# Kernel tuning notes

Measured on AMD Instinct MI355X. Metric: run time of the kernel, lower is better.

The kernel has to match this reference:

```python
import jax, jax.numpy as jnp
import numpy as np

N, T, L = 4, 2048, 2048
DQIN, DFEAT, DQK, DV = 32, 34, 64, 64  # modality feat=34 -> V input = 34-2 = 32, K input = last col


def _sorted_timeline(k, shape):
    return jnp.sort(jax.random.uniform(k, shape, jnp.float32) * 100.0, axis=-1)


def setup_inputs() -> dict:
    key = jax.random.key(0)
    ks = jax.random.split(key, 32)
    inp = {}
    inp["ref_data"] = jax.random.normal(ks[0], (N, 1, T, DQIN), jnp.float32)
    inp["ref_t"] = _sorted_timeline(ks[1], (N, 1, T))
    inp["m1_data"] = jax.random.normal(ks[2], (N, 1, L, DFEAT), jnp.float32)
    inp["m1_t"] = _sorted_timeline(ks[3], (N, 1, L))
    inp["m2_data"] = jax.random.normal(ks[4], (N, 1, L, DFEAT), jnp.float32)
    inp["m2_t"] = _sorted_timeline(ks[5], (N, 1, L))
    inp["m3_data"] = jax.random.normal(ks[6], (N, 1, L, DFEAT), jnp.float32)
    inp["m3_t"] = _sorted_timeline(ks[7], (N, 1, L))
    # shared W_Q (bias=False): d_q_in -> d_qk
    inp["Wq"] = jax.random.normal(ks[8], (DQIN, DQK), jnp.float32) / np.sqrt(DQIN)
    # per-modality params: W_K: 1 -> d_qk (with bias), W_V: (DFEAT-2) -> d_v (with bias), log-temperature
    for i, m in enumerate(["1", "2", "3"]):
        b = 9 + 4 * i
        inp["Wk" + m] = jax.random.normal(ks[b], (1, DQK), jnp.float32)
        inp["bk" + m] = jax.random.normal(ks[b + 1], (DQK,), jnp.float32) * 0.02
        inp["Wv" + m] = jax.random.normal(ks[b + 2], (DFEAT - 2, DV), jnp.float32) / np.sqrt(DFEAT - 2)
        inp["bv" + m] = jax.random.normal(ks[b + 3], (DV,), jnp.float32) * 0.02
        inp["log_tau" + m] = jnp.zeros((), jnp.float32)  # log(init_tau=1)
    return inp


def _unimodal(Q, ref_t, data, t, Wk, bk, Wv, bv, log_tau):
    # K path: last feature column through linear, then feature_map_k = [1, -x]
    Kr = data[..., -1:] @ Wk + bk                                   # (N,1,L,DQK)
    K = jnp.concatenate([jnp.ones(Kr.shape[:-1] + (1,), Kr.dtype), -Kr], axis=-1)  # (N,1,L,DQK+1)
    V = data[..., :-2] @ Wv + bv                                    # (N,1,L,DV)
    tau = jnp.exp(log_tau)
    # gaussian weight: -(Q.K)^2 / tau
    S = -jnp.square(jnp.einsum('nhtc,nhlc->nhtl', Q, K)) / tau       # (N,1,T,L)
    mask = (ref_t[..., :, None] >= t[..., None, :]).astype(S.dtype)  # (N,1,T,L)
    A = jax.nn.softmax(S * mask, axis=-1) * mask
    return jnp.einsum('nhtl,nhlc->nhtc', A, V)                       # (N,1,T,DV)


def reference(ref_data, ref_t, m1_data, m1_t, m2_data, m2_t, m3_data, m3_t,
              Wq, Wk1, bk1, Wv1, bv1, log_tau1, Wk2, bk2, Wv2, bv2, log_tau2,
              Wk3, bk3, Wv3, bv3, log_tau3):
    # compute_Q (qk_type='time'): Q = add_one(W_Q(ref_data)) -> append ones column
    Qr = jnp.einsum('nhtd,dk->nhtk', ref_data, Wq)
    Q = jnp.concatenate([Qr, jnp.ones(Qr.shape[:-1] + (1,), Qr.dtype)], axis=-1)  # (N,1,T,DQK+1)
    y1 = _unimodal(Q, ref_t, m1_data, m1_t, Wk1, bk1, Wv1, bv1, log_tau1)
    y2 = _unimodal(Q, ref_t, m2_data, m2_t, Wk2, bk2, Wv2, bv2, log_tau2)
    y3 = _unimodal(Q, ref_t, m3_data, m3_t, Wk3, bk3, Wv3, bv3, log_tau3)
    # original returns dict {m1: y1, m2: y2, m3: y3}; stacked here (3,N,1,T,DV)
    return jnp.stack([y1, y2, y3], axis=0)
```

## Files before the change

### kernel.cpp

```cpp
#include <hip/hip_runtime.h>

namespace {

typedef unsigned int uint;
typedef unsigned short ushort_t;
typedef __attribute__((ext_vector_type(8))) short bf16x8;
typedef __attribute__((ext_vector_type(4))) float f32x4;

constexpr int N = 4, T = 2048, L = 2048;
constexpr int DQIN = 32, DQK = 64;

constexpr int VI_SZ = 3 * N * 64 * L;
constexpr int X_SZ = 3 * N * L;
constexpr int A_SZ = 3 * N * T;

union PK8 { int i[4]; bf16x8 s; };

__global__ __launch_bounds__(256) void mm_prep(
    const float* __restrict__ ref_data, const float* __restrict__ ref_t,
    const float* __restrict__ d1, const float* __restrict__ t1,
    const float* __restrict__ d2, const float* __restrict__ t2,
    const float* __restrict__ d3, const float* __restrict__ t3,
    const float* __restrict__ Wq,
    const float* __restrict__ Wk1, const float* __restrict__ bk1,
    const float* __restrict__ Wv1, const float* __restrict__ bv1, const float* __restrict__ lt1,
    const float* __restrict__ Wk2, const float* __restrict__ bk2,
    const float* __restrict__ Wv2, const float* __restrict__ bv2, const float* __restrict__ lt2,
    const float* __restrict__ Wk3, const float* __restrict__ bk3,
    const float* __restrict__ Wv3, const float* __restrict__ bv3, const float* __restrict__ lt3,
    float* __restrict__ Aq, float* __restrict__ Gq, int* __restrict__ Cq,
    ushort_t* __restrict__ VI, float* __restrict__ X) {
  const int b = blockIdx.x;
  const int tid = threadIdx.x;

  if (b < 32) {
    __shared__ float sWq[DQIN * DQK];
    __shared__ float sWk[3][DQK];
    __shared__ float sbk[3][DQK];
    for (int i = tid; i < DQIN * DQK; i += 256) sWq[i] = Wq[i];
    if (tid < DQK) {
      sWk[0][tid] = Wk1[tid]; sWk[1][tid] = Wk2[tid]; sWk[2][tid] = Wk3[tid];
      sbk[0][tid] = bk1[tid]; sbk[1][tid] = bk2[tid]; sbk[2][tid] = bk3[tid];
    }
    __syncthreads();
    const int idx = b * 256 + tid;
    float x[DQIN];
    const float* rp = ref_data + idx * DQIN;
#pragma unroll
    for (int i = 0; i < DQIN; i++) x[i] = rp[i];
    float qr[DQK];
#pragma unroll
    for (int j = 0; j < DQK; j += 4) {
      float4 acc4 = make_float4(0.f, 0.f, 0.f, 0.f);
#pragma unroll
      for (int i = 0; i < DQIN; i++) {
        const float4 w = *(const float4*)&sWq[i * DQK + j];
        acc4.x = fmaf(x[i], w.x, acc4.x);
        acc4.y = fmaf(x[i], w.y, acc4.y);
        acc4.z = fmaf(x[i], w.z, acc4.z);
        acc4.w = fmaf(x[i], w.w, acc4.w);
      }
      qr[j] = acc4.x; qr[j + 1] = acc4.y; qr[j + 2] = acc4.z; qr[j + 3] = acc4.w;
    }
    const float rs[3] = {__expf(-0.5f * lt1[0]), __expf(-0.5f * lt2[0]), __expf(-0.5f * lt3[0])};
#pragma unroll
    for (int m = 0; m < 3; m++) {
      float g = 0.f, h = 0.f;
#pragma unroll
      for (int j = 1; j < DQK; j++) {
        g = fmaf(qr[j], sWk[m][j - 1], g);
        h = fmaf(qr[j], sbk[m][j - 1], h);
      }
      g += sWk[m][DQK - 1];
      h += sbk[m][DQK - 1];
      Aq[m * (N * T) + idx] = (qr[0] - h) * rs[m];
      Gq[m * (N * T) + idx] = g * rs[m];
    }
  } else if (b < 128) {
    const int sidx = (b - 32) * 256 + tid;
    const int m = sidx >> 13;
    const int nt = sidx & 8191;
    const int n = nt >> 11;
    const float rt = ref_t[nt];
    const float* tml = ((m == 0) ? t1 : (m == 1 ? t2 : t3)) + n * L;
    int lo = 0, hi = L;
    while (lo < hi) {
      const int mid = (lo + hi) >> 1;
      if (tml[mid] <= rt) lo = mid + 1; else hi = mid;
    }
    Cq[m * 8192 + nt] = lo;
  } else {
    const int vb = b - 128;
    const int mn = vb >> 5;
    const int m = mn >> 2, n = mn & 3;
    const int lseg0 = (vb & 31) * 64;
    const float* dm = (m == 0) ? d1 : (m == 1 ? d2 : d3);
    const float* Wv = (m == 0) ? Wv1 : (m == 1 ? Wv2 : Wv3);
    const float* bv = (m == 0) ? bv1 : (m == 1 ? bv2 : bv3);
    const int cdim = tid & 63;
    const int qq = tid >> 6;
    const int l0 = lseg0 + qq * 16;

    float Wc[32];
#pragma unroll
    for (int i = 0; i < 32; i++) Wc[i] = Wv[i * 64 + cdim];
    const float bvc = bv[cdim];

    uint hi16[16], lo16[16];
#pragma unroll 4
    for (int k = 0; k < 16; k++) {
      const float* dp = dm + (size_t)(n * L + l0 + k) * 34;
      float acc = bvc;
#pragma unroll
      for (int i = 0; i < 32; i++) acc = fmaf(dp[i], Wc[i], acc);
      uint u = __float_as_uint(acc);
      uint h = (u + 0x7fffu + ((u >> 16) & 1u)) & 0xffff0000u;
      float res = acc - __uint_as_float(h);
      uint ul = __float_as_uint(res);
      uint hl = (ul + 0x7fffu + ((ul >> 16) & 1u)) >> 16;
      hi16[k] = h >> 16;
      lo16[k] = hl;
    }
    int pkh[8], pkl[8];
#pragma unroll
    for (int p = 0; p < 8; p++) {
      pkh[p] = (int)(hi16[2 * p] | (hi16[2 * p + 1] << 16));
      pkl[p] = (int)(lo16[2 * p] | (lo16[2 * p + 1] << 16));
    }
    ushort_t* dst = VI + (size_t)(mn * 64 + cdim) * (2 * L) + (l0 >> 3) * 16;
    *(int4*)dst = make_int4(pkh[0], pkh[1], pkh[2], pkh[3]);
    *(int4*)(dst + 8) = make_int4(pkl[0], pkl[1], pkl[2], pkl[3]);
    *(int4*)(dst + 16) = make_int4(pkh[4], pkh[5], pkh[6], pkh[7]);
    *(int4*)(dst + 24) = make_int4(pkl[4], pkl[5], pkl[6], pkl[7]);

    if (tid < 64) {
      const int l = lseg0 + tid;
      X[mn * L + l] = dm[(size_t)(n * L + l) * 34 + 33];
    }
  }
}

__device__ inline void stage_chunk(ushort_t* dstbuf, const ushort_t* VIb, int ch,
                                   int w, int lane) {
#pragma unroll
  for (int i = 0; i < 4; i++) {
    const int u = w * 256 + i * 64 + lane;
    const int rr = u >> 4;
    const int gs = u & 15;
    const int g = (gs - rr) & 15;
    const ushort_t* src = VIb + (size_t)rr * 4096 + ch * 128 + g * 8;
    __builtin_amdgcn_global_load_lds(
        (const __attribute__((address_space(1))) void*)src,
        (__attribute__((address_space(3))) void*)(dstbuf + (size_t)(w * 256 + i * 64) * 8),
        16, 0, 0);
  }
}

__global__ __launch_bounds__(256) void mm_attn_main(
    const ushort_t* __restrict__ VI, const float* __restrict__ X,
    const float* __restrict__ Aq, const float* __restrict__ Gq, const int* __restrict__ Cq,
    float* __restrict__ out) {
  __shared__ ushort_t sbuf[2][8192];

  const int b = blockIdx.x;
  const int mn = b % 12;
  const int r = b / 12;
  const int rg = (r & 1) ? (r >> 1) : (127 - (r >> 1));
  const int tbase = mn * T + rg * 16;

  const int tid = threadIdx.x;
  const int lane = tid & 63;
  const int w = tid >> 6;
  const int q = lane >> 4;
  const int m16 = lane & 15;

  const int c = Cq[tbase + m16];
  const int cmax = __shfl(c, 15, 64);
  const int cmin = __shfl(c, 0, 64);
  const int nch = (cmax + 63) >> 6;

  float a = 0.f, g = 0.f;
  if (nch > 0) { a = Aq[tbase + m16]; g = Gq[tbase + m16]; }

  f32x4 acc = (f32x4){0.f, 0.f, 0.f, 0.f};
  float z = 0.f;

  const ushort_t* VIb = VI + (size_t)mn * 64 * 4096;
  const float* xp = X + mn * L;
  const int rdim = w * 16 + m16;

  if (nch > 0) stage_chunk(sbuf[0], VIb, 0, w, lane);
  __syncthreads();

  for (int ch = 0; ch < nch; ch++) {
    const int nb = ch & 1;
    if (ch + 1 < nch) stage_chunk(sbuf[nb ^ 1], VIb, ch + 1, w, lane);

    const int base = ch << 6;
    const ushort_t* buf = sbuf[nb];
#pragma unroll
    for (int hh = 0; hh < 2; hh++) {
      const int k0 = base + hh * 32 + q * 8;
      const float4 xa = *(const float4*)&xp[k0];
      const float4 xb = *(const float4*)&xp[k0 + 4];
      const float xs[8] = {xa.x, xa.y, xa.z, xa.w, xb.x, xb.y, xb.z, xb.w};
      float wv[8];
      if (base + hh * 32 + 32 <= cmin) {
#pragma unroll
        for (int j = 0; j < 8; j++) {
          const float d = fmaf(-g, xs[j], a);
          wv[j] = __expf(-d * d);
          z += wv[j];
        }
      } else {
#pragma unroll
        for (int j = 0; j < 8; j++) {
          const float d = fmaf(-g, xs[j], a);
          const float e = __expf(-d * d);
          wv[j] = (k0 + j < c) ? e : 0.f;
          z += wv[j];
        }
      }
      PK8 ph, pl;
#pragma unroll
      for (int p2 = 0; p2 < 4; p2++) {
        const uint u0 = __float_as_uint(wv[2 * p2]);
        const uint u1 = __float_as_uint(wv[2 * p2 + 1]);
        const uint h0 = u0 & 0xffff0000u, h1 = u1 & 0xffff0000u;
        const float l0f = wv[2 * p2] - __uint_as_float(h0);
        const float l1f = wv[2 * p2 + 1] - __uint_as_float(h1);
        ph.i[p2] = (int)((h0 >> 16) | h1);
        pl.i[p2] = (int)((__float_as_uint(l0f) >> 16) | (__float_as_uint(l1f) & 0xffff0000u));
      }
      const bf16x8 ahi = ph.s, alo = pl.s;
      const int g0 = (hh * 4 + q) * 2;
      const int uih = rdim * 16 + ((g0 + rdim) & 15);
      const int uil = rdim * 16 + ((g0 + 1 + rdim) & 15);
      const bf16x8 bh = *(const bf16x8*)&buf[(size_t)uih * 8];
      const bf16x8 bl = *(const bf16x8*)&buf[(size_t)uil * 8];
      acc = __builtin_amdgcn_mfma_f32_16x16x32_bf16(ahi, bh, acc, 0, 0, 0);
      acc = __builtin_amdgcn_mfma_f32_16x16x32_bf16(ahi, bl, acc, 0, 0, 0);
      acc = __builtin_amdgcn_mfma_f32_16x16x32_bf16(alo, bh, acc, 0, 0, 0);
    }
    __syncthreads();
  }

  z += __shfl_xor(z, 16, 64);
  z += __shfl_xor(z, 32, 64);

#pragma unroll
  for (int rr2 = 0; rr2 < 4; rr2++) {
    const int row = q * 4 + rr2;
    const float zr = __shfl(z, row, 64);
    const int cr = __shfl(c, row, 64);
    const float inv = 1.0f / (zr + (float)(L - cr));
    out[(size_t)(tbase + row) * 64 + w * 16 + m16] = acc[rr2] * inv;
  }
}

}

extern "C" void kernel_launch(void* const* d_in, const int* in_sizes, int n_in,
                              void* d_out, int out_size, void* d_ws, size_t ws_size,
                              hipStream_t stream) {
  const float* ref_data = (const float*)d_in[0];
  const float* ref_t = (const float*)d_in[1];
  const float* m1_data = (const float*)d_in[2];
  const float* m1_t = (const float*)d_in[3];
  const float* m2_data = (const float*)d_in[4];
  const float* m2_t = (const float*)d_in[5];
  const float* m3_data = (const float*)d_in[6];
  const float* m3_t = (const float*)d_in[7];
  const float* Wq = (const float*)d_in[8];
  const float* Wk1 = (const float*)d_in[9];
  const float* bk1 = (const float*)d_in[10];
  const float* Wv1 = (const float*)d_in[11];
  const float* bv1 = (const float*)d_in[12];
  const float* lt1 = (const float*)d_in[13];
  const float* Wk2 = (const float*)d_in[14];
  const float* bk2 = (const float*)d_in[15];
  const float* Wv2 = (const float*)d_in[16];
  const float* bv2 = (const float*)d_in[17];
  const float* lt2 = (const float*)d_in[18];
  const float* Wk3 = (const float*)d_in[19];
  const float* bk3 = (const float*)d_in[20];
  const float* Wv3 = (const float*)d_in[21];
  const float* bv3 = (const float*)d_in[22];
  const float* lt3 = (const float*)d_in[23];

  float* ws = (float*)d_ws;
  ushort_t* VI = (ushort_t*)ws;
  float* Xw = ws + VI_SZ;
  float* Aq = Xw + X_SZ;
  float* Gq = Aq + A_SZ;
  int* Cq = (int*)(Gq + A_SZ);

  mm_prep<<<dim3(512), dim3(256), 0, stream>>>(
      ref_data, ref_t, m1_data, m1_t, m2_data, m2_t, m3_data, m3_t, Wq,
      Wk1, bk1, Wv1, bv1, lt1, Wk2, bk2, Wv2, bv2, lt2, Wk3, bk3, Wv3, bv3, lt3,
      Aq, Gq, Cq, VI, Xw);
  mm_attn_main<<<dim3(12 * 128), dim3(256), 0, stream>>>(
      VI, Xw, Aq, Gq, Cq, (float*)d_out);
}
```

Measured before the change: 174.8 us.

## Compute each row tile's weights once per wave and pair early/late tiles per block

The main attention kernel now has each wave cover all 64 output columns with four MFMA accumulators. Previously the four waves in a block each recomputed the same exp weights for a 16-row tile. Each 128-thread block now holds two waves that process a causally short tile and its mirrored long tile, sharing the staged V chunks, with the long tile's chunk count driving the loop. The prep kernel's Q-side work is also split across modalities into three times as many blocks for more parallelism. This cuts redundant transcendental work and balances work per block, but lowers threads per block and raises per-thread register pressure.

```diff
diff --git a/kernel.cpp b/kernel.cpp
--- a/kernel.cpp
+++ b/kernel.cpp
@@ -33,17 +33,18 @@
   const int b = blockIdx.x;
   const int tid = threadIdx.x;
 
-  if (b < 32) {
+  if (b < 96) {
+    const int m = b >> 5;
+    const int idx = (b & 31) * 256 + tid;
     __shared__ float sWq[DQIN * DQK];
-    __shared__ float sWk[3][DQK];
-    __shared__ float sbk[3][DQK];
+    __shared__ float sWk[DQK];
+    __shared__ float sbk[DQK];
+    const float* Wk = (m == 0) ? Wk1 : (m == 1 ? Wk2 : Wk3);
+    const float* bk = (m == 0) ? bk1 : (m == 1 ? bk2 : bk3);
+    const float* lt = (m == 0) ? lt1 : (m == 1 ? lt2 : lt3);
     for (int i = tid; i < DQIN * DQK; i += 256) sWq[i] = Wq[i];
-    if (tid < DQK) {
-      sWk[0][tid] = Wk1[tid]; sWk[1][tid] = Wk2[tid]; sWk[2][tid] = Wk3[tid];
-      sbk[0][tid] = bk1[tid]; sbk[1][tid] = bk2[tid]; sbk[2][tid] = bk3[tid];
-    }
+    if (tid < DQK) { sWk[tid] = Wk[tid]; sbk[tid] = bk[tid]; }
     __syncthreads();
-    const int idx = b * 256 + tid;
     float x[DQIN];
     const float* rp = ref_data + idx * DQIN;
 #pragma unroll
@@ -62,22 +63,19 @@
       }
       qr[j] = acc4.x; qr[j + 1] = acc4.y; qr[j + 2] = acc4.z; qr[j + 3] = acc4.w;
     }
-    const float rs[3] = {__expf(-0.5f * lt1[0]), __expf(-0.5f * lt2[0]), __expf(-0.5f * lt3[0])};
-#pragma unroll
-    for (int m = 0; m < 3; m++) {
-      float g = 0.f, h = 0.f;
-#pragma unroll
-      for (int j = 1; j < DQK; j++) {
-        g = fmaf(qr[j], sWk[m][j - 1], g);
-        h = fmaf(qr[j], sbk[m][j - 1], h);
-      }
-      g += sWk[m][DQK - 1];
-      h += sbk[m][DQK - 1];
-      Aq[m * (N * T) + idx] = (qr[0] - h) * rs[m];
-      Gq[m * (N * T) + idx] = g * rs[m];
-    }
-  } else if (b < 128) {
-    const int sidx = (b - 32) * 256 + tid;
+    const float rs = __expf(-0.5f * lt[0]);
+    float g = 0.f, h = 0.f;
+#pragma unroll
+    for (int j = 1; j < DQK; j++) {
+      g = fmaf(qr[j], sWk[j - 1], g);
+      h = fmaf(qr[j], sbk[j - 1], h);
+    }
+    g += sWk[DQK - 1];
+    h += sbk[DQK - 1];
+    Aq[m * (N * T) + idx] = (qr[0] - h) * rs;
+    Gq[m * (N * T) + idx] = g * rs;
+  } else if (b < 192) {
+    const int sidx = (b - 96) * 256 + tid;
     const int m = sidx >> 13;
     const int nt = sidx & 8191;
     const int n = nt >> 11;
@@ -90,7 +88,7 @@
     }
     Cq[m * 8192 + nt] = lo;
   } else {
-    const int vb = b - 128;
+    const int vb = b - 192;
     const int mn = vb >> 5;
     const int m = mn >> 2, n = mn & 3;
     const int lseg0 = (vb & 31) * 64;
@@ -143,20 +141,20 @@
 __device__ inline void stage_chunk(ushort_t* dstbuf, const ushort_t* VIb, int ch,
                                    int w, int lane) {
 #pragma unroll
-  for (int i = 0; i < 4; i++) {
-    const int u = w * 256 + i * 64 + lane;
+  for (int i = 0; i < 8; i++) {
+    const int u = w * 512 + i * 64 + lane;
     const int rr = u >> 4;
     const int gs = u & 15;
     const int g = (gs - rr) & 15;
     const ushort_t* src = VIb + (size_t)rr * 4096 + ch * 128 + g * 8;
     __builtin_amdgcn_global_load_lds(
         (const __attribute__((address_space(1))) void*)src,
-        (__attribute__((address_space(3))) void*)(dstbuf + (size_t)(w * 256 + i * 64) * 8),
+        (__attribute__((address_space(3))) void*)(dstbuf + (size_t)(w * 512 + i * 64) * 8),
         16, 0, 0);
   }
 }
 
-__global__ __launch_bounds__(256) void mm_attn_main(
+__global__ __launch_bounds__(128) void mm_attn_main(
     const ushort_t* __restrict__ VI, const float* __restrict__ X,
     const float* __restrict__ Aq, const float* __restrict__ Gq, const int* __restrict__ Cq,
     float* __restrict__ out) {
@@ -164,9 +162,7 @@
 
   const int b = blockIdx.x;
   const int mn = b % 12;
-  const int r = b / 12;
-  const int rg = (r & 1) ? (r >> 1) : (127 - (r >> 1));
-  const int tbase = mn * T + rg * 16;
+  const int k = b / 12;
 
   const int tid = threadIdx.x;
   const int lane = tid & 63;
@@ -174,73 +170,87 @@
   const int q = lane >> 4;
   const int m16 = lane & 15;
 
+  const int rg = (w == 0) ? k : (127 - k);
+  const int tbase = mn * T + rg * 16;
+
   const int c = Cq[tbase + m16];
   const int cmax = __shfl(c, 15, 64);
   const int cmin = __shfl(c, 0, 64);
   const int nch = (cmax + 63) >> 6;
 
-  float a = 0.f, g = 0.f;
-  if (nch > 0) { a = Aq[tbase + m16]; g = Gq[tbase + m16]; }
-
-  f32x4 acc = (f32x4){0.f, 0.f, 0.f, 0.f};
+  const int cB = Cq[mn * T + (127 - k) * 16 + 15];
+  const int nchB = (cB + 63) >> 6;
+
+  const float a = Aq[tbase + m16];
+  const float g = Gq[tbase + m16];
+
+  f32x4 acc[4];
+#pragma unroll
+  for (int ct = 0; ct < 4; ct++) acc[ct] = (f32x4){0.f, 0.f, 0.f, 0.f};
   float z = 0.f;
 
   const ushort_t* VIb = VI + (size_t)mn * 64 * 4096;
   const float* xp = X + mn * L;
-  const int rdim = w * 16 + m16;
-
-  if (nch > 0) stage_chunk(sbuf[0], VIb, 0, w, lane);
+
+  stage_chunk(sbuf[0], VIb, 0, w, lane);
   __syncthreads();
 
-  for (int ch = 0; ch < nch; ch++) {
+  for (int ch = 0; ch < nchB; ch++) {
     const int nb = ch & 1;
-    if (ch + 1 < nch) stage_chunk(sbuf[nb ^ 1], VIb, ch + 1, w, lane);
-
-    const int base = ch << 6;
-    const ushort_t* buf = sbuf[nb];
-#pragma unroll
-    for (int hh = 0; hh < 2; hh++) {
-      const int k0 = base + hh * 32 + q * 8;
-      const float4 xa = *(const float4*)&xp[k0];
-      const float4 xb = *(const float4*)&xp[k0 + 4];
-      const float xs[8] = {xa.x, xa.y, xa.z, xa.w, xb.x, xb.y, xb.z, xb.w};
-      float wv[8];
-      if (base + hh * 32 + 32 <= cmin) {
-#pragma unroll
-        for (int j = 0; j < 8; j++) {
-          const float d = fmaf(-g, xs[j], a);
-          wv[j] = __expf(-d * d);
-          z += wv[j];
+    if (ch + 1 < nchB) stage_chunk(sbuf[nb ^ 1], VIb, ch + 1, w, lane);
+
+    if (ch < nch) {
+      const int base = ch << 6;
+      const ushort_t* buf = sbuf[nb];
+      const bool inter = (base + 64 <= cmin);
+#pragma unroll
+      for (int kk = 0; kk < 2; kk++) {
+        const int k0 = base + kk * 32 + q * 8;
+        const float4 xa = *(const float4*)&xp[k0];
+        const float4 xb = *(const float4*)&xp[k0 + 4];
+        const float xs[8] = {xa.x, xa.y, xa.z, xa.w, xb.x, xb.y, xb.z, xb.w};
+        float wv[8];
+        if (inter) {
+#pragma unroll
+          for (int j = 0; j < 8; j++) {
+            const float d = fmaf(-g, xs[j], a);
+            wv[j] = __expf(-d * d);
+            z += wv[j];
+          }
+        } else {
+#pragma unroll
+          for (int j = 0; j < 8; j++) {
+            const float d = fmaf(-g, xs[j], a);
+            const float e = __expf(-d * d);
+            wv[j] = (k0 + j < c) ? e : 0.f;
+            z += wv[j];
+          }
         }
-      } else {
-#pragma unroll
-        for (int j = 0; j < 8; j++) {
-          const float d = fmaf(-g, xs[j], a);
-          const float e = __expf(-d * d);
-          wv[j] = (k0 + j < c) ? e : 0.f;
-          z += wv[j];
+        PK8 ph, pl;
+#pragma unroll
+        for (int p2 = 0; p2 < 4; p2++) {
+          const uint u0 = __float_as_uint(wv[2 * p2]);
+          const uint u1 = __float_as_uint(wv[2 * p2 + 1]);
+          const uint h0 = u0 & 0xffff0000u, h1 = u1 & 0xffff0000u;
+          const float l0f = wv[2 * p2] - __uint_as_float(h0);
+          const float l1f = wv[2 * p2 + 1] - __uint_as_float(h1);
+          ph.i[p2] = (int)((h0 >> 16) | h1);
+          pl.i[p2] = (int)((__float_as_uint(l0f) >> 16) | (__float_as_uint(l1f) & 0xffff0000u));
+        }
+        const bf16x8 ahi = ph.s, alo = pl.s;
+#pragma unroll
+        for (int ct = 0; ct < 4; ct++) {
+          const int r = ct * 16 + m16;
+          const int go = (kk * 4 + q) * 2;
+          const int uih = r * 16 + ((go + r) & 15);
+          const int uil = r * 16 + ((go + 1 + r) & 15);
+          const bf16x8 bh = *(const bf16x8*)&buf[(size_t)uih * 8];
+          const bf16x8 bl = *(const bf16x8*)&buf[(size_t)uil * 8];
+          acc[ct] = __builtin_amdgcn_mfma_f32_16x16x32_bf16(ahi, bh, acc[ct], 0, 0, 0);
+          acc[ct] = __builtin_amdgcn_mfma_f32_16x16x32_bf16(ahi, bl, acc[ct], 0, 0, 0);
+          acc[ct] = __builtin_amdgcn_mfma_f32_16x16x32_bf16(alo, bh, acc[ct], 0, 0, 0);
         }
       }
-      PK8 ph, pl;
-#pragma unroll
-      for (int p2 = 0; p2 < 4; p2++) {
-        const uint u0 = __float_as_uint(wv[2 * p2]);
-        const uint u1 = __float_as_uint(wv[2 * p2 + 1]);
-        const uint h0 = u0 & 0xffff0000u, h1 = u1 & 0xffff0000u;
-        const float l0f = wv[2 * p2] - __uint_as_float(h0);
-        const float l1f = wv[2 * p2 + 1] - __uint_as_float(h1);
-        ph.i[p2] = (int)((h0 >> 16) | h1);
-        pl.i[p2] = (int)((__float_as_uint(l0f) >> 16) | (__float_as_uint(l1f) & 0xffff0000u));
-      }
-      const bf16x8 ahi = ph.s, alo = pl.s;
-      const int g0 = (hh * 4 + q) * 2;
-      const int uih = rdim * 16 + ((g0 + rdim) & 15);
-      const int uil = rdim * 16 + ((g0 + 1 + rdim) & 15);
-      const bf16x8 bh = *(const bf16x8*)&buf[(size_t)uih * 8];
-      const bf16x8 bl = *(const bf16x8*)&buf[(size_t)uil * 8];
-      acc = __builtin_amdgcn_mfma_f32_16x16x32_bf16(ahi, bh, acc, 0, 0, 0);
-      acc = __builtin_amdgcn_mfma_f32_16x16x32_bf16(ahi, bl, acc, 0, 0, 0);
-      acc = __builtin_amdgcn_mfma_f32_16x16x32_bf16(alo, bh, acc, 0, 0, 0);
     }
     __syncthreads();
   }
@@ -249,12 +259,15 @@
   z += __shfl_xor(z, 32, 64);
 
 #pragma unroll
-  for (int rr2 = 0; rr2 < 4; rr2++) {
-    const int row = q * 4 + rr2;
+  for (int rr = 0; rr < 4; rr++) {
+    const int row = q * 4 + rr;
     const float zr = __shfl(z, row, 64);
     const int cr = __shfl(c, row, 64);
     const float inv = 1.0f / (zr + (float)(L - cr));
-    out[(size_t)(tbase + row) * 64 + w * 16 + m16] = acc[rr2] * inv;
+#pragma unroll
+    for (int ct = 0; ct < 4; ct++) {
+      out[(size_t)(tbase + row) * 64 + ct * 16 + m16] = acc[ct][rr] * inv;
+    }
   }
 }
 
@@ -295,10 +308,10 @@
   float* Gq = Aq + A_SZ;
   int* Cq = (int*)(Gq + A_SZ);
 
-  mm_prep<<<dim3(512), dim3(256), 0, stream>>>(
+  mm_prep<<<dim3(576), dim3(256), 0, stream>>>(
       ref_data, ref_t, m1_data, m1_t, m2_data, m2_t, m3_data, m3_t, Wq,
       Wk1, bk1, Wv1, bv1, lt1, Wk2, bk2, Wv2, bv2, lt2, Wk3, bk3, Wv3, bv3, lt3,
       Aq, Gq, Cq, VI, Xw);
-  mm_attn_main<<<dim3(12 * 128), dim3(256), 0, stream>>>(
+  mm_attn_main<<<dim3(12 * 64), dim3(128), 0, stream>>>(
       VI, Xw, Aq, Gq, Cq, (float*)d_out);
 }
```

New measurement: 171.2 us. 1.02x faster.
